# Kernel optimization log

Hardware: AMD Instinct MI355X
Metric: run time of the kernel (lower is better)

## Reference

```python
import jax, jax.numpy as jnp
import numpy as np

N = 100000
E = 3200000
IN_DIM = 128
HID = 128
OUT_DIM = 2
L = 3
P = 2
PART = IN_DIM // P  # 64, equals HID // P
G = 64  # number of graphs
EPS = 1e-5


def setup_inputs() -> dict:
    key = jax.random.key(0)
    ks = jax.random.split(key, 12)
    x = jax.random.normal(ks[0], (N, IN_DIM), dtype=jnp.float32)
    edge_index = jax.random.randint(ks[1], (2, E), 0, N, dtype=jnp.int64)
    batch = jnp.sort(jax.random.randint(ks[2], (N,), 0, G, dtype=jnp.int64))
    # stacked GCNConv params: all convs are PART->PART (64->64)
    W_conv = jax.random.normal(ks[3], (L, P, PART, PART), dtype=jnp.float32) * 0.1
    b_conv = jax.random.normal(ks[4], (L, P, PART), dtype=jnp.float32) * 0.02
    # batchnorm (eval mode, running stats)
    bn_gamma = jnp.ones((L, HID), dtype=jnp.float32) + 0.1 * jax.random.normal(ks[5], (L, HID))
    bn_beta = 0.1 * jax.random.normal(ks[6], (L, HID), dtype=jnp.float32)
    bn_mean = 0.1 * jax.random.normal(ks[7], (L, HID), dtype=jnp.float32)
    bn_var = jnp.ones((L, HID), dtype=jnp.float32) + 0.1 * jax.random.uniform(ks[8], (L, HID))
    W_fc1 = jax.random.normal(ks[9], (HID * L, HID), dtype=jnp.float32) * 0.05
    b_fc1 = jnp.zeros((HID,), dtype=jnp.float32)
    W_fc2 = jax.random.normal(ks[10], (HID, OUT_DIM), dtype=jnp.float32) * 0.05
    b_fc2 = jnp.zeros((OUT_DIM,), dtype=jnp.float32)
    return dict(x=x, edge_index=edge_index, batch=batch, W_conv=W_conv, b_conv=b_conv,
                bn_gamma=bn_gamma, bn_beta=bn_beta, bn_mean=bn_mean, bn_var=bn_var,
                W_fc1=W_fc1, b_fc1=b_fc1, W_fc2=W_fc2, b_fc2=b_fc2)


def _gcn_norm(edge_index, num_nodes):
    # add self loops, compute symmetric normalization (PyG gcn_norm, edge_weight=1)
    loop = jnp.arange(num_nodes, dtype=edge_index.dtype)
    row = jnp.concatenate([edge_index[0], loop])  # source j
    col = jnp.concatenate([edge_index[1], loop])  # target i
    deg = jax.ops.segment_sum(jnp.ones_like(col, dtype=jnp.float32), col, num_segments=num_nodes)
    dis = jnp.where(deg > 0, jax.lax.rsqrt(jnp.maximum(deg, 1.0)), 0.0)
    norm = dis[row] * dis[col]  # [E+N]
    return row, col, norm


def _gcn_conv(xp, W, b, row, col, norm, num_nodes):
    xw = xp @ W                               # [N, PART] linear first (PyG GCNConv)
    msg = xw[row] * norm[:, None]             # gather + scale
    out = jax.ops.segment_sum(msg, col, num_segments=num_nodes)  # scatter-add
    return out + b


def reference(x, edge_index, batch, W_conv, b_conv, bn_gamma, bn_beta, bn_mean, bn_var,
              W_fc1, b_fc1, W_fc2, b_fc2):
    num_nodes = x.shape[0]
    row, col, norm = _gcn_norm(edge_index, num_nodes)
    layer_outputs = []
    h = x
    for l in range(L):
        parts = jnp.split(h, P, axis=-1)
        outs = [_gcn_conv(parts[p], W_conv[l, p], b_conv[l, p], row, col, norm, num_nodes)
                for p in range(P)]
        h = jnp.concatenate(outs, axis=-1)  # [N, HID]
        # BatchNorm1d in eval mode
        h = (h - bn_mean[l]) * jax.lax.rsqrt(bn_var[l] + EPS) * bn_gamma[l] + bn_beta[l]
        h = jax.nn.relu(h)  # dropout inactive in eval
        layer_outputs.append(h)
    hjk = jnp.concatenate(layer_outputs, axis=-1)  # [N, HID*L]
    # global mean pool per graph
    sums = jax.ops.segment_sum(hjk, batch, num_segments=G)
    cnts = jax.ops.segment_sum(jnp.ones((num_nodes,), dtype=jnp.float32), batch, num_segments=G)
    pooled = sums / jnp.maximum(cnts, 1.0)[:, None]  # [G, HID*L]
    z = jax.nn.relu(pooled @ W_fc1 + b_fc1)
    z = z @ W_fc2 + b_fc2
    return jax.nn.log_softmax(z, axis=-1)
```

## Files before the change

kernel.cpp:

```cpp
#include <hip/hip_runtime.h>
#include <cstdint>
#include <cstddef>

#define FEAT 128
#define NLAYERS 3
#define EPS 1e-5f
#define TILE 8192
#define SBSHIFT 9

typedef unsigned int uint32;
typedef float floatx2 __attribute__((ext_vector_type(2)));

__device__ __forceinline__ uint32 pack_bf16(float a, float b) {
  uint32 ua = __float_as_uint(a);
  uint32 ub = __float_as_uint(b);
  ua += 0x7fffu + ((ua >> 16) & 1u);
  ub += 0x7fffu + ((ub >> 16) & 1u);
  return (ua >> 16) | (ub & 0xffff0000u);
}

__global__ void scan1(const int* __restrict__ in, int* __restrict__ bsum, int n) {
  __shared__ int s[256];
  int t = threadIdx.x;
  int i = blockIdx.x * 256 + t;
  s[t] = (i < n) ? in[i] : 0;
  __syncthreads();
  for (int o = 128; o > 0; o >>= 1) {
    if (t < o) s[t] += s[t + o];
    __syncthreads();
  }
  if (t == 0) bsum[blockIdx.x] = s[0];
}

__global__ void scan2(int* __restrict__ bsum, int nb) {
  __shared__ int s[512];
  int t = threadIdx.x;
  int v = (t < nb) ? bsum[t] : 0;
  s[t] = v;
  __syncthreads();
  for (int o = 1; o < 512; o <<= 1) {
    int add = (t >= o) ? s[t - o] : 0;
    __syncthreads();
    s[t] += add;
    __syncthreads();
  }
  if (t < nb) bsum[t] = s[t] - v;
}

__global__ void gscan3(const int* __restrict__ in, const int* __restrict__ bsum,
                       int* __restrict__ out, int n) {
  __shared__ int s[256];
  int t = threadIdx.x;
  int i = blockIdx.x * 256 + t;
  int v = (i < n) ? in[i] : 0;
  s[t] = v;
  __syncthreads();
  for (int o = 1; o < 256; o <<= 1) {
    int add = (t >= o) ? s[t - o] : 0;
    __syncthreads();
    s[t] += add;
    __syncthreads();
  }
  if (i < n) out[i] = bsum[blockIdx.x] + s[t] - v;
}

__global__ __launch_bounds__(256) void l1count_k(const int* __restrict__ col,
                                                 int* __restrict__ C, int E, int NT,
                                                 int SB) {
  __shared__ int h[256];
  int t = threadIdx.x;
  h[t] = 0;
  __syncthreads();
  int base = blockIdx.x * TILE;
  int end = min(base + TILE, E);
  for (int i = base + t; i < end; i += 256) atomicAdd(&h[col[i] >> SBSHIFT], 1);
  __syncthreads();
  if (t < SB) C[t * NT + blockIdx.x] = h[t];
}

__global__ __launch_bounds__(256) void l1scatter_k(const int* __restrict__ row,
                                                   const int* __restrict__ col,
                                                   const int* __restrict__ Cex,
                                                   uint32* __restrict__ bbuf, int E, int NT,
                                                   int SB) {
  __shared__ int cur[256];
  int t = threadIdx.x;
  if (t < SB) cur[t] = Cex[t * NT + blockIdx.x];
  __syncthreads();
  int base = blockIdx.x * TILE;
  int end = min(base + TILE, E);
  for (int i = base + t; i < end; i += 256) {
    int c = col[i];
    int pos = atomicAdd(&cur[c >> SBSHIFT], 1);
    bbuf[pos] = ((uint32)(c & ((1 << SBSHIFT) - 1)) << 17) | (uint32)row[i];
  }
}

__global__ __launch_bounds__(256) void l2_k(const uint32* __restrict__ bbuf,
                                            const int* __restrict__ Cex,
                                            int* __restrict__ rowstart,
                                            float* __restrict__ dis,
                                            int* __restrict__ csrc,
                                            int N, int E, int NT, int SB) {
  __shared__ int hist[512];
  __shared__ int scanbuf[256];
  const int b = blockIdx.x;
  const int t = threadIdx.x;
  const int n0 = b << SBSHIFT;
  hist[t] = 0;
  hist[t + 256] = 0;
  __syncthreads();
  const int s = Cex[b * NT];
  const int e1 = (b == SB - 1) ? E : Cex[(b + 1) * NT];
  for (int i = s + t; i < e1; i += 256) {
    atomicAdd(&hist[bbuf[i] >> 17], 1);
  }
  __syncthreads();
  int a0 = hist[2 * t];
  int a1 = hist[2 * t + 1];
  int pair = a0 + a1;
  scanbuf[t] = pair;
  __syncthreads();
  for (int o = 1; o < 256; o <<= 1) {
    int add = (t >= o) ? scanbuf[t - o] : 0;
    __syncthreads();
    scanbuf[t] += add;
    __syncthreads();
  }
  int pairExcl = scanbuf[t] - pair;
  int c0 = s + pairExcl;
  int c1 = c0 + a0;
  int n = n0 + 2 * t;
  if (n < N) {
    rowstart[n] = c0;
    dis[n] = rsqrtf((float)(a0 + 1));
  }
  if (n + 1 < N) {
    rowstart[n + 1] = c1;
    dis[n + 1] = rsqrtf((float)(a1 + 1));
  }
  if (b == SB - 1 && t == 0) rowstart[N] = E;
  hist[2 * t] = c0;
  hist[2 * t + 1] = c1;
  __syncthreads();
  for (int i = s + t; i < e1; i += 256) {
    uint32 pk = bbuf[i];
    int pos = atomicAdd(&hist[pk >> 17], 1);
    csrc[pos] = (int)(pk & 0x1FFFFu);
  }
}

__global__ void boundaries_k(const int* __restrict__ batch, int* __restrict__ gstart,
                             int N, int G) {
  int n = blockIdx.x * blockDim.x + threadIdx.x;
  if (n >= N) return;
  int b = batch[n];
  int prev = (n == 0) ? -1 : batch[n - 1];
  for (int g = prev + 1; g <= b; ++g) gstart[g] = n;
  if (n == N - 1) {
    for (int g = b + 1; g <= G; ++g) gstart[g] = N;
  }
}

__global__ void bnprep_k(const float* __restrict__ bconv, const float* __restrict__ gamma,
                         const float* __restrict__ beta, const float* __restrict__ mean,
                         const float* __restrict__ var, float* __restrict__ bns,
                         float* __restrict__ bnt) {
  int l = blockIdx.x;
  int f = threadIdx.x;
  int i = l * FEAT + f;
  float s = gamma[i] * rsqrtf(var[i] + EPS);
  bns[i] = s;
  bnt[i] = (bconv[i] - mean[i]) * s + beta[i];
}

__global__ __launch_bounds__(256) void xw_k(const void* __restrict__ h, int isBf16,
                                            const float* __restrict__ W,
                                            const float* __restrict__ dis,
                                            uint32* __restrict__ xs8, int N) {
  __shared__ float hT[64 * 68];
  __shared__ float Ws[64 * 64];
  const int t = threadIdx.x;
  const int a = t >> 4;
  const int b = t & 15;
  const int base = blockIdx.x * 64;

  for (int p = 0; p < 2; ++p) {
    {
      const float4* src = (const float4*)(W + p * 4096);
      float4* dst = (float4*)Ws;
#pragma unroll
      for (int r = 0; r < 4; ++r) dst[r * 256 + t] = src[r * 256 + t];
    }
#pragma unroll
    for (int r = 0; r < 4; ++r) {
      int qid = r * 256 + t;
      int n = qid >> 4;
      int q = qid & 15;
      float4 v = make_float4(0.f, 0.f, 0.f, 0.f);
      int node = base + n;
      if (node < N) {
        if (isBf16) {
          uint2 wv = *(const uint2*)((const uint32*)h + (size_t)node * 64 + p * 32 + q * 2);
          v.x = __uint_as_float(wv.x << 16);
          v.y = __uint_as_float(wv.x & 0xffff0000u);
          v.z = __uint_as_float(wv.y << 16);
          v.w = __uint_as_float(wv.y & 0xffff0000u);
        } else {
          v = *(const float4*)((const float*)h + (size_t)node * FEAT + p * 64 + q * 4);
        }
      }
      hT[(q * 4 + 0) * 68 + n] = v.x;
      hT[(q * 4 + 1) * 68 + n] = v.y;
      hT[(q * 4 + 2) * 68 + n] = v.z;
      hT[(q * 4 + 3) * 68 + n] = v.w;
    }
    __syncthreads();

    float acc[4][4];
#pragma unroll
    for (int i = 0; i < 4; ++i)
#pragma unroll
      for (int j = 0; j < 4; ++j) acc[i][j] = 0.f;

#pragma unroll 8
    for (int k = 0; k < 64; ++k) {
      float4 hv = *(const float4*)(hT + k * 68 + a * 4);
      float4 wv = *(const float4*)(Ws + k * 64 + b * 4);
      acc[0][0] += hv.x * wv.x; acc[0][1] += hv.x * wv.y; acc[0][2] += hv.x * wv.z; acc[0][3] += hv.x * wv.w;
      acc[1][0] += hv.y * wv.x; acc[1][1] += hv.y * wv.y; acc[1][2] += hv.y * wv.z; acc[1][3] += hv.y * wv.w;
      acc[2][0] += hv.z * wv.x; acc[2][1] += hv.z * wv.y; acc[2][2] += hv.z * wv.z; acc[2][3] += hv.z * wv.w;
      acc[3][0] += hv.w * wv.x; acc[3][1] += hv.w * wv.y; acc[3][2] += hv.w * wv.z; acc[3][3] += hv.w * wv.w;
    }

#pragma unroll
    for (int i = 0; i < 4; ++i) {
      int node = base + a * 4 + i;
      if (node < N) {
        float d = dis[node];
        int w = __builtin_amdgcn_cvt_pk_fp8_f32(acc[i][0] * d, acc[i][1] * d, 0, false);
        w = __builtin_amdgcn_cvt_pk_fp8_f32(acc[i][2] * d, acc[i][3] * d, w, true);
        xs8[(size_t)node * 32 + p * 16 + b] = (uint32)w;
      }
    }
    __syncthreads();
  }
}

__global__ __launch_bounds__(256) void gather_k(const unsigned short* __restrict__ xs8,
                                                const float* __restrict__ dis,
                                                const int* __restrict__ rowstart,
                                                const int* __restrict__ csrc,
                                                const int* __restrict__ batch,
                                                const float* __restrict__ bns,
                                                const float* __restrict__ bnt,
                                                uint32* __restrict__ hout,
                                                float* __restrict__ sums,
                                                int layer, int N) {
  const int w = threadIdx.x >> 6;
  const int lane = threadIdx.x & 63;
  const int wid = blockIdx.x * 4 + w;
  const bool valid = (wid < N);
  const int f = lane * 2;

  float rx = 0.f, ry = 0.f;
  int g = -1;

  if (valid) {
    int e0 = rowstart[wid];
    int e1 = rowstart[wid + 1];
    float di = dis[wid];

    int selfv = xs8[(size_t)wid * 64 + lane];
    floatx2 sc = __builtin_amdgcn_cvt_pk_f32_fp8(selfv, false);
    float ax = sc[0];
    float ay = sc[1];

    for (int base = e0; base < e1; base += 64) {
      int cnt = min(64, e1 - base);
      int my = (lane < cnt) ? csrc[base + lane] : 0;
      int j = 0;
      for (; j + 7 < cnt; j += 8) {
        int s0 = __shfl(my, j);
        int s1 = __shfl(my, j + 1);
        int s2 = __shfl(my, j + 2);
        int s3 = __shfl(my, j + 3);
        int s4 = __shfl(my, j + 4);
        int s5 = __shfl(my, j + 5);
        int s6 = __shfl(my, j + 6);
        int s7 = __shfl(my, j + 7);
        int v0 = xs8[(size_t)s0 * 64 + lane];
        int v1 = xs8[(size_t)s1 * 64 + lane];
        int v2 = xs8[(size_t)s2 * 64 + lane];
        int v3 = xs8[(size_t)s3 * 64 + lane];
        int v4 = xs8[(size_t)s4 * 64 + lane];
        int v5 = xs8[(size_t)s5 * 64 + lane];
        int v6 = xs8[(size_t)s6 * 64 + lane];
        int v7 = xs8[(size_t)s7 * 64 + lane];
        floatx2 c0 = __builtin_amdgcn_cvt_pk_f32_fp8(v0, false);
        floatx2 c1 = __builtin_amdgcn_cvt_pk_f32_fp8(v1, false);
        floatx2 c2 = __builtin_amdgcn_cvt_pk_f32_fp8(v2, false);
        floatx2 c3 = __builtin_amdgcn_cvt_pk_f32_fp8(v3, false);
        floatx2 c4 = __builtin_amdgcn_cvt_pk_f32_fp8(v4, false);
        floatx2 c5 = __builtin_amdgcn_cvt_pk_f32_fp8(v5, false);
        floatx2 c6 = __builtin_amdgcn_cvt_pk_f32_fp8(v6, false);
        floatx2 c7 = __builtin_amdgcn_cvt_pk_f32_fp8(v7, false);
        ax += c0[0] + c1[0] + c2[0] + c3[0] + c4[0] + c5[0] + c6[0] + c7[0];
        ay += c0[1] + c1[1] + c2[1] + c3[1] + c4[1] + c5[1] + c6[1] + c7[1];
      }
      for (; j < cnt; ++j) {
        int s = __shfl(my, j);
        int v = xs8[(size_t)s * 64 + lane];
        floatx2 c = __builtin_amdgcn_cvt_pk_f32_fp8(v, false);
        ax += c[0];
        ay += c[1];
      }
    }
    ax *= di;
    ay *= di;
    rx = fmaxf(ax * bns[f] + bnt[f], 0.f);
    ry = fmaxf(ay * bns[f + 1] + bnt[f + 1], 0.f);
    if (hout) hout[(size_t)wid * 64 + lane] = pack_bf16(rx, ry);
    g = batch[wid];
  }

  __shared__ float ps[4][FEAT];
  __shared__ int gs[4];
  if (lane == 0) gs[w] = g;
  *(float2*)&ps[w][f] = make_float2(rx, ry);
  __syncthreads();
  if (gs[0] >= 0 && gs[0] == gs[1] && gs[1] == gs[2] && gs[2] == gs[3]) {
    int t = threadIdx.x;
    if (t < FEAT) {
      float s = ps[0][t] + ps[1][t] + ps[2][t] + ps[3][t];
      atomicAdd(&sums[(size_t)gs[0] * (NLAYERS * FEAT) + layer * FEAT + t], s);
    }
  } else if (valid) {
    float* sp = sums + (size_t)g * (NLAYERS * FEAT) + layer * FEAT + f;
    atomicAdd(sp, rx);
    atomicAdd(sp + 1, ry);
  }
}

__global__ __launch_bounds__(128) void head_k(const float* __restrict__ sums,
                                              const int* __restrict__ gstart,
                                              const float* __restrict__ W1,
                                              const float* __restrict__ b1,
                                              const float* __restrict__ W2,
                                              const float* __restrict__ b2,
                                              float* __restrict__ out) {
  __shared__ float pooled[NLAYERS * FEAT];
  __shared__ float z1[FEAT];
  __shared__ float z2[2];
  int g = blockIdx.x;
  int t = threadIdx.x;
  float cnt = (float)(gstart[g + 1] - gstart[g]);
  float inv = 1.f / fmaxf(cnt, 1.f);
  for (int k = t; k < NLAYERS * FEAT; k += 128) pooled[k] = sums[g * (NLAYERS * FEAT) + k] * inv;
  __syncthreads();
  float acc = b1[t];
  for (int k = 0; k < NLAYERS * FEAT; ++k) acc += pooled[k] * W1[k * FEAT + t];
  z1[t] = fmaxf(acc, 0.f);
  __syncthreads();
  if (t < 2) {
    float a = b2[t];
    for (int j = 0; j < FEAT; ++j) a += z1[j] * W2[j * 2 + t];
    z2[t] = a;
  }
  __syncthreads();
  if (t < 2) {
    float m = fmaxf(z2[0], z2[1]);
    float lse = m + logf(expf(z2[0] - m) + expf(z2[1] - m));
    out[g * 2 + t] = z2[t] - lse;
  }
}


extern "C" void kernel_launch(void* const* d_in, const int* in_sizes, int n_in,
                              void* d_out, int out_size, void* d_ws, size_t ws_size,
                              hipStream_t stream) {
  const float* x    = (const float*)d_in[0];
  const int*   ei   = (const int*)d_in[1];
  const int*   batch= (const int*)d_in[2];
  const float* Wc   = (const float*)d_in[3];
  const float* bc   = (const float*)d_in[4];
  const float* gam  = (const float*)d_in[5];
  const float* bet  = (const float*)d_in[6];
  const float* mu   = (const float*)d_in[7];
  const float* var  = (const float*)d_in[8];
  const float* W1   = (const float*)d_in[9];
  const float* b1   = (const float*)d_in[10];
  const float* W2   = (const float*)d_in[11];
  const float* b2   = (const float*)d_in[12];
  float* out = (float*)d_out;

  const int N = in_sizes[0] / FEAT;
  const int E = in_sizes[1] / 2;
  const int G = out_size / 2;
  const int SB = (N + (1 << SBSHIFT) - 1) >> SBSHIFT;
  const int NT = (E + TILE - 1) / TILE;

  const int* row = ei;
  const int* col = ei + E;

  char* p = (char*)d_ws;
  auto alloc = [&](size_t bytes) -> void* {
    void* q = (void*)p;
    p += (bytes + 255) & ~(size_t)255;
    return q;
  };
  float*  dis      = (float*)alloc((size_t)N * 4);
  int*    rowstart = (int*)alloc((size_t)(N + 1) * 4);
  int*    csrc     = (int*)alloc((size_t)E * 4);
  int*    bsum     = (int*)alloc(1024 * 4);
  int*    gstart   = (int*)alloc(1024 * 4);
  int*    C        = (int*)alloc((size_t)256 * NT * 4);
  float*  bns      = (float*)alloc(NLAYERS * FEAT * 4);
  float*  bnt      = (float*)alloc(NLAYERS * FEAT * 4);
  float*  sums     = (float*)alloc((size_t)G * NLAYERS * FEAT * 4);
  uint32* bufA     = (uint32*)alloc((size_t)N * FEAT);
  uint32* bufB     = (uint32*)alloc((size_t)N * 64 * 4);
  uint32* bbuf     = (uint32*)bufB;

  const int nbN = (N + 255) / 256;
  const int Csz = SB * NT;
  const int nbC = (Csz + 255) / 256;

  hipMemsetAsync(sums, 0, (size_t)G * NLAYERS * FEAT * 4, stream);

  l1count_k<<<NT, 256, 0, stream>>>(col, C, E, NT, SB);
  scan1<<<nbC, 256, 0, stream>>>(C, bsum, Csz);
  scan2<<<1, 512, 0, stream>>>(bsum, nbC);
  gscan3<<<nbC, 256, 0, stream>>>(C, bsum, C, Csz);
  l1scatter_k<<<NT, 256, 0, stream>>>(row, col, C, bbuf, E, NT, SB);
  l2_k<<<SB, 256, 0, stream>>>(bbuf, C, rowstart, dis, csrc, N, E, NT, SB);

  boundaries_k<<<nbN, 256, 0, stream>>>(batch, gstart, N, G);
  bnprep_k<<<NLAYERS, FEAT, 0, stream>>>(bc, gam, bet, mu, var, bns, bnt);

  const int xwBlocks = (N + 63) / 64;
  const int gaBlocks = (N + 3) / 4;
  const void* hin = (const void*)x;
  int isBf16 = 0;
  for (int l = 0; l < NLAYERS; ++l) {
    xw_k<<<xwBlocks, 256, 0, stream>>>(hin, isBf16, Wc + (size_t)l * 8192, dis, bufA, N);
    uint32* hptr = (l == NLAYERS - 1) ? nullptr : bufB;
    gather_k<<<gaBlocks, 256, 0, stream>>>((const unsigned short*)bufA, dis, rowstart,
                                           csrc, batch, bns + l * FEAT, bnt + l * FEAT,
                                           hptr, sums, l, N);
    hin = (const void*)bufB;
    isBf16 = 1;
  }

  head_k<<<G, 128, 0, stream>>>(sums, gstart, W1, b1, W2, b2, out);
}
```

Before: 638.3 us.

## Fuse prep kernels, widen gather blocks and unroll, enlarge bucketing tile

```diff
diff --git a/kernel.cpp b/kernel.cpp
--- a/kernel.cpp
+++ b/kernel.cpp
@@ -5,7 +5,7 @@
 #define FEAT 128
 #define NLAYERS 3
 #define EPS 1e-5f
-#define TILE 8192
+#define TILE 16384
 #define SBSHIFT 9
 
 typedef unsigned int uint32;
@@ -150,9 +150,27 @@
   }
 }
 
-__global__ void boundaries_k(const int* __restrict__ batch, int* __restrict__ gstart,
-                             int N, int G) {
-  int n = blockIdx.x * blockDim.x + threadIdx.x;
+__global__ __launch_bounds__(256) void prep_k(const int* __restrict__ batch,
+                                              int* __restrict__ gstart,
+                                              const float* __restrict__ bconv,
+                                              const float* __restrict__ gamma,
+                                              const float* __restrict__ beta,
+                                              const float* __restrict__ mean,
+                                              const float* __restrict__ var,
+                                              float* __restrict__ bns,
+                                              float* __restrict__ bnt,
+                                              int N, int G) {
+  int t = threadIdx.x;
+  if (blockIdx.x < NLAYERS) {
+    if (t < FEAT) {
+      int i = blockIdx.x * FEAT + t;
+      float s = gamma[i] * rsqrtf(var[i] + EPS);
+      bns[i] = s;
+      bnt[i] = (bconv[i] - mean[i]) * s + beta[i];
+    }
+    return;
+  }
+  int n = (blockIdx.x - NLAYERS) * 256 + t;
   if (n >= N) return;
   int b = batch[n];
   int prev = (n == 0) ? -1 : batch[n - 1];
@@ -160,18 +178,6 @@
   if (n == N - 1) {
     for (int g = b + 1; g <= G; ++g) gstart[g] = N;
   }
-}
-
-__global__ void bnprep_k(const float* __restrict__ bconv, const float* __restrict__ gamma,
-                         const float* __restrict__ beta, const float* __restrict__ mean,
-                         const float* __restrict__ var, float* __restrict__ bns,
-                         float* __restrict__ bnt) {
-  int l = blockIdx.x;
-  int f = threadIdx.x;
-  int i = l * FEAT + f;
-  float s = gamma[i] * rsqrtf(var[i] + EPS);
-  bns[i] = s;
-  bnt[i] = (bconv[i] - mean[i]) * s + beta[i];
 }
 
 __global__ __launch_bounds__(256) void xw_k(const void* __restrict__ h, int isBf16,
@@ -247,7 +253,7 @@
   }
 }
 
-__global__ __launch_bounds__(256) void gather_k(const unsigned short* __restrict__ xs8,
+__global__ __launch_bounds__(512) void gather_k(const unsigned short* __restrict__ xs8,
                                                 const float* __restrict__ dis,
                                                 const int* __restrict__ rowstart,
                                                 const int* __restrict__ csrc,
@@ -259,7 +265,7 @@
                                                 int layer, int N) {
   const int w = threadIdx.x >> 6;
   const int lane = threadIdx.x & 63;
-  const int wid = blockIdx.x * 4 + w;
+  const int wid = blockIdx.x * 8 + w;
   const bool valid = (wid < N);
   const int f = lane * 2;
 
@@ -280,33 +286,33 @@
       int cnt = min(64, e1 - base);
       int my = (lane < cnt) ? csrc[base + lane] : 0;
       int j = 0;
-      for (; j + 7 < cnt; j += 8) {
-        int s0 = __shfl(my, j);
-        int s1 = __shfl(my, j + 1);
-        int s2 = __shfl(my, j + 2);
-        int s3 = __shfl(my, j + 3);
-        int s4 = __shfl(my, j + 4);
-        int s5 = __shfl(my, j + 5);
-        int s6 = __shfl(my, j + 6);
-        int s7 = __shfl(my, j + 7);
-        int v0 = xs8[(size_t)s0 * 64 + lane];
-        int v1 = xs8[(size_t)s1 * 64 + lane];
-        int v2 = xs8[(size_t)s2 * 64 + lane];
-        int v3 = xs8[(size_t)s3 * 64 + lane];
-        int v4 = xs8[(size_t)s4 * 64 + lane];
-        int v5 = xs8[(size_t)s5 * 64 + lane];
-        int v6 = xs8[(size_t)s6 * 64 + lane];
-        int v7 = xs8[(size_t)s7 * 64 + lane];
-        floatx2 c0 = __builtin_amdgcn_cvt_pk_f32_fp8(v0, false);
-        floatx2 c1 = __builtin_amdgcn_cvt_pk_f32_fp8(v1, false);
-        floatx2 c2 = __builtin_amdgcn_cvt_pk_f32_fp8(v2, false);
-        floatx2 c3 = __builtin_amdgcn_cvt_pk_f32_fp8(v3, false);
-        floatx2 c4 = __builtin_amdgcn_cvt_pk_f32_fp8(v4, false);
-        floatx2 c5 = __builtin_amdgcn_cvt_pk_f32_fp8(v5, false);
-        floatx2 c6 = __builtin_amdgcn_cvt_pk_f32_fp8(v6, false);
-        floatx2 c7 = __builtin_amdgcn_cvt_pk_f32_fp8(v7, false);
-        ax += c0[0] + c1[0] + c2[0] + c3[0] + c4[0] + c5[0] + c6[0] + c7[0];
-        ay += c0[1] + c1[1] + c2[1] + c3[1] + c4[1] + c5[1] + c6[1] + c7[1];
+      for (; j + 15 < cnt; j += 16) {
+        int ss[16];
+        int vv[16];
+#pragma unroll
+        for (int u = 0; u < 16; ++u) ss[u] = __shfl(my, j + u);
+#pragma unroll
+        for (int u = 0; u < 16; ++u) vv[u] = xs8[(size_t)ss[u] * 64 + lane];
+#pragma unroll
+        for (int u = 0; u < 16; ++u) {
+          floatx2 c = __builtin_amdgcn_cvt_pk_f32_fp8(vv[u], false);
+          ax += c[0];
+          ay += c[1];
+        }
+      }
+      for (; j + 3 < cnt; j += 4) {
+        int ss[4];
+        int vv[4];
+#pragma unroll
+        for (int u = 0; u < 4; ++u) ss[u] = __shfl(my, j + u);
+#pragma unroll
+        for (int u = 0; u < 4; ++u) vv[u] = xs8[(size_t)ss[u] * 64 + lane];
+#pragma unroll
+        for (int u = 0; u < 4; ++u) {
+          floatx2 c = __builtin_amdgcn_cvt_pk_f32_fp8(vv[u], false);
+          ax += c[0];
+          ay += c[1];
+        }
       }
       for (; j < cnt; ++j) {
         int s = __shfl(my, j);
@@ -324,15 +330,20 @@
     g = batch[wid];
   }
 
-  __shared__ float ps[4][FEAT];
-  __shared__ int gs[4];
+  __shared__ float ps[8][FEAT];
+  __shared__ int gs[8];
   if (lane == 0) gs[w] = g;
   *(float2*)&ps[w][f] = make_float2(rx, ry);
   __syncthreads();
-  if (gs[0] >= 0 && gs[0] == gs[1] && gs[1] == gs[2] && gs[2] == gs[3]) {
+  bool same = (gs[0] >= 0);
+#pragma unroll
+  for (int i = 1; i < 8; ++i) same = same && (gs[i] == gs[0]);
+  if (same) {
     int t = threadIdx.x;
     if (t < FEAT) {
-      float s = ps[0][t] + ps[1][t] + ps[2][t] + ps[3][t];
+      float s = 0.f;
+#pragma unroll
+      for (int i = 0; i < 8; ++i) s += ps[i][t];
       atomicAdd(&sums[(size_t)gs[0] * (NLAYERS * FEAT) + layer * FEAT + t], s);
     }
   } else if (valid) {
@@ -435,17 +446,17 @@
   l1scatter_k<<<NT, 256, 0, stream>>>(row, col, C, bbuf, E, NT, SB);
   l2_k<<<SB, 256, 0, stream>>>(bbuf, C, rowstart, dis, csrc, N, E, NT, SB);
 
-  boundaries_k<<<nbN, 256, 0, stream>>>(batch, gstart, N, G);
-  bnprep_k<<<NLAYERS, FEAT, 0, stream>>>(bc, gam, bet, mu, var, bns, bnt);
+  prep_k<<<NLAYERS + nbN, 256, 0, stream>>>(batch, gstart, bc, gam, bet, mu, var,
+                                            bns, bnt, N, G);
 
   const int xwBlocks = (N + 63) / 64;
-  const int gaBlocks = (N + 3) / 4;
+  const int gaBlocks = (N + 7) / 8;
   const void* hin = (const void*)x;
   int isBf16 = 0;
   for (int l = 0; l < NLAYERS; ++l) {
     xw_k<<<xwBlocks, 256, 0, stream>>>(hin, isBf16, Wc + (size_t)l * 8192, dis, bufA, N);
     uint32* hptr = (l == NLAYERS - 1) ? nullptr : bufB;
-    gather_k<<<gaBlocks, 256, 0, stream>>>((const unsigned short*)bufA, dis, rowstart,
+    gather_k<<<gaBlocks, 512, 0, stream>>>((const unsigned short*)bufA, dis, rowstart,
                                            csrc, batch, bns + l * FEAT, bnt + l * FEAT,
                                            hptr, sums, l, N);
     hin = (const void*)bufB;
```

Result: no change. 649.6 us (+1.8%).
